# Optimization experiments

Hardware: AMD Instinct MI355X
Metric: run time of the kernel (lower is better)

The kernel has to match this reference:

```python
import jax, jax.numpy as jnp
import numpy as np

D_MODEL = 1024
HEADS = 16
D_K = D_MODEL // HEADS
B, S = 2, 2048
NEG = -1e9


def setup_inputs() -> dict:
    key = jax.random.key(0)
    ks = jax.random.split(key, 12)
    sc = 1.0 / np.sqrt(D_MODEL)
    inp = {
        'query': jax.random.normal(ks[0], (B, S, D_MODEL), jnp.float32),
        'key': jax.random.normal(ks[1], (B, S, D_MODEL), jnp.float32),
        'value': jax.random.normal(ks[2], (B, S, D_MODEL), jnp.float32),
        'mask': jnp.tril(jnp.ones((S, S), jnp.int32))[None, None],  # [1,1,S,S] causal
        'Wq': jax.random.normal(ks[3], (D_MODEL, D_MODEL), jnp.float32) * sc,
        'bq': jax.random.normal(ks[4], (D_MODEL,), jnp.float32) * 0.02,
        'Wk': jax.random.normal(ks[5], (D_MODEL, D_MODEL), jnp.float32) * sc,
        'bk': jax.random.normal(ks[6], (D_MODEL,), jnp.float32) * 0.02,
        'Wv': jax.random.normal(ks[7], (D_MODEL, D_MODEL), jnp.float32) * sc,
        'bv': jax.random.normal(ks[8], (D_MODEL,), jnp.float32) * 0.02,
        'Wo': jax.random.normal(ks[9], (D_MODEL, D_MODEL), jnp.float32) * sc,
        'bo': jax.random.normal(ks[10], (D_MODEL,), jnp.float32) * 0.02,
    }
    return inp


def reference(query, key, value, mask, Wq, bq, Wk, bk, Wv, bv, Wo, bo):
    # QKV projections (torch Linear: x @ W.T + b; here W stored as [in,out])
    def split_heads(x):  # [B,S,D] -> [B,H,S,dk]
        return x.reshape(B, S, HEADS, D_K).transpose(0, 2, 1, 3)

    q = split_heads(query @ Wq + bq)
    k = split_heads(key @ Wk + bk)
    v = split_heads(value @ Wv + bv)

    scores = jnp.einsum('bhqd,bhkd->bhqk', q, k) / np.sqrt(D_K)
    scores = jnp.where(mask == 0, NEG, scores)
    attn = jax.nn.softmax(scores, axis=-1)  # dropout p=0 (eval) -> identity
    out = jnp.einsum('bhqk,bhkd->bhqd', attn, v)
    out = out.transpose(0, 2, 1, 3).reshape(B, S, D_MODEL)
    return out @ Wo + bo
```

## Files before the change

kernel.cpp:

```cpp
#include <hip/hip_runtime.h>
#include <hip/hip_bf16.h>
#include <cstdint>
#include <cstddef>

typedef short short8 __attribute__((ext_vector_type(8)));
typedef float f32x4 __attribute__((ext_vector_type(4)));
typedef float f32x16 __attribute__((ext_vector_type(16)));

#define SS 2048
#define DK 64
#define LAMBDA 0.18033688011112042f

__device__ __forceinline__ float b2f(ushort u) {
    union { uint32_t i; float f; } x; x.i = ((uint32_t)u) << 16; return x.f;
}
__device__ __forceinline__ ushort f2b(float f) {
    union { float f; uint32_t i; } x; x.f = f;
    uint32_t r = (x.i + 0x7fffu + ((x.i >> 16) & 1u)) >> 16;
    return (ushort)r;
}
__device__ __forceinline__ uint32_t pk_bf16(float a, float b) {
    union { __hip_bfloat162 v; uint32_t u; } x;
    float2 f2; f2.x = a; f2.y = b;
    x.v = __float22bfloat162_rn(f2);
    return x.u;
}

__device__ __forceinline__ void gl_lds16(const ushort* __restrict__ g, ushort* l) {
    __builtin_amdgcn_global_load_lds(
        (const __attribute__((address_space(1))) uint32_t*)(uintptr_t)g,
        (__attribute__((address_space(3))) uint32_t*)(uintptr_t)l, 16, 0, 0);
}

__device__ __forceinline__ bool probe_bf16(const uint32_t* __restrict__ probe) {
    const int lane = threadIdx.x & 63;
    int c = 0;
#pragma unroll
    for (int i = 0; i < 4; ++i) {
        uint32_t u = probe[lane * 4 + i];
        uint32_t e = (u >> 7) & 0xffu;
        c += (e >= 100u && e <= 140u) ? 1 : 0;
    }
    unsigned long long b = __ballot(c >= 3);
    return __popcll(b) > 32;
}

__device__ __forceinline__ void ld8_f32_to_bf16(ushort* dst, const float* __restrict__ src) {
    float4 a = *(const float4*)src;
    float4 b = *(const float4*)(src + 4);
    ushort t[8] = {f2b(a.x), f2b(a.y), f2b(a.z), f2b(a.w),
                   f2b(b.x), f2b(b.y), f2b(b.z), f2b(b.w)};
    *(uint4*)dst = *(uint4*)t;
}

__global__ __launch_bounds__(256) void transpose_all(const void* __restrict__ W0,
                                                     const void* __restrict__ W1,
                                                     const void* __restrict__ W2,
                                                     const void* __restrict__ W3,
                                                     ushort* __restrict__ ws,
                                                     const uint32_t* __restrict__ probe,
                                                     size_t wotOff) {
    __shared__ __align__(16) ushort t[64 * 72];
    const bool isbf = probe_bf16(probe);
    const int z = blockIdx.z;
    const void* W = (z == 0) ? W0 : (z == 1) ? W1 : (z == 2) ? W2 : W3;
    ushort* T = ws + ((z < 3) ? ((size_t)z << 20) : wotOff);

    const int n0 = blockIdx.x * 64, k0 = blockIdx.y * 64;
    const int tid = threadIdx.x;
    const int r = tid >> 3, cg = (tid & 7) * 8;
    if (isbf) {
        const ushort* Wb = (const ushort*)W;
#pragma unroll
        for (int p = 0; p < 2; ++p) {
            int k = r + p * 32;
            *(uint4*)&t[k * 72 + cg] = *(const uint4*)&Wb[(size_t)(k0 + k) * 1024 + n0 + cg];
        }
    } else {
        const float* Wf = (const float*)W;
#pragma unroll
        for (int p = 0; p < 2; ++p) {
            int k = r + p * 32;
            ld8_f32_to_bf16(&t[k * 72 + cg], &Wf[(size_t)(k0 + k) * 1024 + n0 + cg]);
        }
    }
    __syncthreads();
#pragma unroll
    for (int p = 0; p < 2; ++p) {
        int n = r + p * 32;
        uint4 o;
        ushort* op = (ushort*)&o;
#pragma unroll
        for (int i = 0; i < 8; ++i) op[i] = t[(cg + i) * 72 + n];
        *(uint4*)&T[(size_t)(n0 + n) * 1024 + k0 + cg] = o;
    }
}

__global__ __launch_bounds__(256) void conv_qkv(const void* __restrict__ q,
                                                const void* __restrict__ k,
                                                const void* __restrict__ v,
                                                ushort* __restrict__ ws,
                                                const uint32_t* __restrict__ probe,
                                                size_t dstOff) {
    const bool isbf = probe_bf16(probe);
    const int z = blockIdx.y;
    const void* src = (z == 0) ? q : (z == 1) ? k : v;
    ushort* dst = ws + dstOff + ((size_t)z << 22);
    const size_t i = ((size_t)blockIdx.x * 256 + threadIdx.x) * 8;
    if (isbf)
        *(uint4*)&dst[i] = *(const uint4*)&((const ushort*)src)[i];
    else
        ld8_f32_to_bf16(&dst[i], &((const float*)src)[i]);
}

template <int PRE>
__global__ __launch_bounds__(256) void qkv_gemm(const void* __restrict__ qp,
                                                const void* __restrict__ kp,
                                                const void* __restrict__ vp,
                                                const void* __restrict__ bqp,
                                                const void* __restrict__ bkp,
                                                const void* __restrict__ bvp,
                                                ushort* __restrict__ ws,
                                                const uint32_t* __restrict__ probe) {
    __shared__ __align__(16) ushort As[2][128 * 32];
    __shared__ __align__(16) ushort Bs[2][128 * 32];
    const bool isbf = probe_bf16(probe);
    const int z = blockIdx.z;
    const ushort* Bt = ws + ((size_t)z << 20);
    const void* bias = (z == 0) ? bqp : (z == 1) ? bkp : bvp;
    ushort* C = ws + ((size_t)((PRE ? 16 : 5) + 4 * z) << 20);
    const float scl = (z == 0) ? LAMBDA : 1.0f;

    const int tid = threadIdx.x;
    const int lane = tid & 63, wid = tid >> 6;
    const int l15 = lane & 15, g = lane >> 4;
    const int wm = wid >> 1, wn = wid & 1;
    const int id0 = blockIdx.y * 8 + blockIdx.x;
    const int id = (id0 & 7) * 32 + (id0 >> 3);
    const int m0 = (id >> 3) * 128, n0 = (id & 7) * 128;
    const int sr = tid >> 2, sc = (tid & 3) * 8;
    const int lrow = (lane >> 2), lcol = (lane & 3) * 8;

    f32x4 acc[4][4];
#pragma unroll
    for (int i = 0; i < 4; ++i)
#pragma unroll
        for (int j = 0; j < 4; ++j) {
            f32x4 zz = {0.f, 0.f, 0.f, 0.f};
            acc[i][j] = zz;
        }

    auto stageAB = [&](int kk, int bsel) {
#pragma unroll
        for (int q = 0; q < 2; ++q) {
            const int row = (wid * 2 + q) * 16 + lrow;
            gl_lds16(&Bt[(size_t)(n0 + row) * 1024 + kk + lcol], &Bs[bsel][(wid * 2 + q) * 512]);
        }
        if (PRE) {
            const ushort* Ab = ws + ((size_t)(4 + 4 * z) << 20);
#pragma unroll
            for (int q = 0; q < 2; ++q) {
                const int row = (wid * 2 + q) * 16 + lrow;
                gl_lds16(&Ab[(size_t)(m0 + row) * 1024 + kk + lcol],
                         &As[bsel][(wid * 2 + q) * 512]);
            }
        } else {
            const void* A = (z == 0) ? qp : (z == 1) ? kp : vp;
            if (isbf) {
                const ushort* Ab = (const ushort*)A;
#pragma unroll
                for (int q = 0; q < 2; ++q) {
                    const int row = (wid * 2 + q) * 16 + lrow;
                    gl_lds16(&Ab[(size_t)(m0 + row) * 1024 + kk + lcol],
                             &As[bsel][(wid * 2 + q) * 512]);
                }
            } else {
                const float* Af = (const float*)A;
                ld8_f32_to_bf16(&As[bsel][sr * 32 + sc], &Af[(size_t)(m0 + sr) * 1024 + kk + sc]);
                ld8_f32_to_bf16(&As[bsel][(sr + 64) * 32 + sc],
                                &Af[(size_t)(m0 + sr + 64) * 1024 + kk + sc]);
            }
        }
    };

    stageAB(0, 0);
    __syncthreads();
#pragma unroll 2
    for (int kk = 0; kk < 1024; kk += 32) {
        const int cur = (kk >> 5) & 1;
        if (kk < 1024 - 32) stageAB(kk + 32, cur ^ 1);
        short8 a[4], b[4];
#pragma unroll
        for (int i = 0; i < 4; ++i)
            a[i] = *(const short8*)&As[cur][(wm * 64 + i * 16 + l15) * 32 + g * 8];
#pragma unroll
        for (int j = 0; j < 4; ++j)
            b[j] = *(const short8*)&Bs[cur][(wn * 64 + j * 16 + l15) * 32 + g * 8];
#pragma unroll
        for (int i = 0; i < 4; ++i)
#pragma unroll
            for (int j = 0; j < 4; ++j)
                acc[i][j] = __builtin_amdgcn_mfma_f32_16x16x32_bf16(a[i], b[j], acc[i][j], 0, 0, 0);
        __syncthreads();
    }

#pragma unroll
    for (int i = 0; i < 4; ++i)
#pragma unroll
        for (int j = 0; j < 4; ++j) {
            const int col = n0 + wn * 64 + j * 16 + l15;
            const float bv = isbf ? b2f(((const ushort*)bias)[col]) : ((const float*)bias)[col];
#pragma unroll
            for (int r = 0; r < 4; ++r) {
                const int row = m0 + wm * 64 + i * 16 + g * 4 + r;
                const float v = (acc[i][j][r] + bv) * scl;
                size_t idx;
                if (z != 2) {
                    idx = ((size_t)((row >> 11) * 16 + (col >> 6)) * SS + (row & 2047)) * 64 +
                          (col & 63);
                } else {
                    idx = ((size_t)((row >> 11) * 16 + (col >> 6)) * 64 + (col & 63)) * SS +
                          (row & 2047);
                }
                C[idx] = f2b(v);
            }
        }
}

__global__ __launch_bounds__(256) void out_gemm(const ushort* __restrict__ A,
                                                const ushort* __restrict__ Bt,
                                                const void* __restrict__ bias,
                                                void* __restrict__ C,
                                                const uint32_t* __restrict__ probe) {
    __shared__ __align__(16) ushort As[2][64 * 32];
    __shared__ __align__(16) ushort Bs[2][128 * 32];
    const bool isbf = probe_bf16(probe);
    const int tid = threadIdx.x;
    const int lane = tid & 63, wid = tid >> 6;
    const int l15 = lane & 15, g = lane >> 4;
    const int wm = wid >> 1, wn = wid & 1;
    const int id0 = blockIdx.y * 8 + blockIdx.x;
    const int id = (id0 & 7) * 64 + (id0 >> 3);
    const int m0 = (id >> 3) * 64, n0 = (id & 7) * 128;
    const int lrow = (lane >> 2), lcol = (lane & 3) * 8;

    f32x4 acc[2][4];
#pragma unroll
    for (int i = 0; i < 2; ++i)
#pragma unroll
        for (int j = 0; j < 4; ++j) {
            f32x4 zz = {0.f, 0.f, 0.f, 0.f};
            acc[i][j] = zz;
        }

    auto stageAB = [&](int kk, int bsel) {
        {
            const int row = wid * 16 + lrow;
            gl_lds16(&A[(size_t)(m0 + row) * 1024 + kk + lcol], &As[bsel][wid * 512]);
        }
#pragma unroll
        for (int q = 0; q < 2; ++q) {
            const int row = (wid * 2 + q) * 16 + lrow;
            gl_lds16(&Bt[(size_t)(n0 + row) * 1024 + kk + lcol], &Bs[bsel][(wid * 2 + q) * 512]);
        }
    };

    stageAB(0, 0);
    __syncthreads();
#pragma unroll 2
    for (int kk = 0; kk < 1024; kk += 32) {
        const int cur = (kk >> 5) & 1;
        if (kk < 1024 - 32) stageAB(kk + 32, cur ^ 1);
        short8 a[2], b[4];
#pragma unroll
        for (int i = 0; i < 2; ++i)
            a[i] = *(const short8*)&As[cur][(wm * 32 + i * 16 + l15) * 32 + g * 8];
#pragma unroll
        for (int j = 0; j < 4; ++j)
            b[j] = *(const short8*)&Bs[cur][(wn * 64 + j * 16 + l15) * 32 + g * 8];
#pragma unroll
        for (int i = 0; i < 2; ++i)
#pragma unroll
            for (int j = 0; j < 4; ++j)
                acc[i][j] = __builtin_amdgcn_mfma_f32_16x16x32_bf16(a[i], b[j], acc[i][j], 0, 0, 0);
        __syncthreads();
    }

#pragma unroll
    for (int i = 0; i < 2; ++i)
#pragma unroll
        for (int j = 0; j < 4; ++j) {
            const int col = n0 + wn * 64 + j * 16 + l15;
            const float bv = isbf ? b2f(((const ushort*)bias)[col]) : ((const float*)bias)[col];
#pragma unroll
            for (int r = 0; r < 4; ++r) {
                const int row = m0 + wm * 32 + i * 16 + g * 4 + r;
                const float v = acc[i][j][r] + bv;
                const size_t idx = (size_t)row * 1024 + col;
                if (isbf)
                    ((ushort*)C)[idx] = f2b(v);
                else
                    ((float*)C)[idx] = v;
            }
        }
}

__global__ __launch_bounds__(256, 2) void attn_fwd(const ushort* __restrict__ Q,
                                                   const ushort* __restrict__ K,
                                                   const ushort* __restrict__ Vt,
                                                   ushort* __restrict__ O) {
    __shared__ __align__(16) ushort Ks[2][64 * 64];
    __shared__ __align__(16) ushort Vs[2][64 * 64];

    const int y = blockIdx.y;
    const int s0i = (blockIdx.x + y) & 15;
    const int t = (y & 16) ? (15 - s0i) : s0i;
    const int tid = threadIdx.x;
    const int lane = tid & 63, wid = tid >> 6;
    const int l31 = lane & 31, h = lane >> 5;

    const ushort* Qb = Q + (size_t)y * SS * DK;
    const ushort* Kb = K + (size_t)y * SS * DK;
    const ushort* Vb = Vt + (size_t)y * DK * SS;
    const int b = y >> 4, hh = y & 15;

    const int q0w = t * 128 + wid * 32;
    const int nkt = 2 * t + 2;

    const int srow = lane >> 3;
    const int sgc = ((lane & 7) ^ srow) * 8;

    short8 qf[4];
#pragma unroll
    for (int k4 = 0; k4 < 4; ++k4)
        qf[k4] = *(const short8*)&Qb[(size_t)(q0w + l31) * 64 + k4 * 16 + h * 8];

    int foff[2][4];
#pragma unroll
    for (int aa = 0; aa < 2; ++aa)
#pragma unroll
        for (int k4 = 0; k4 < 4; ++k4)
            foff[aa][k4] = (aa * 32 + l31) * 64 + (((k4 * 2 + h) ^ (l31 & 7)) * 8);

    f32x16 acc[2];
#pragma unroll
    for (int nt = 0; nt < 2; ++nt)
#pragma unroll
        for (int r = 0; r < 16; ++r) acc[nt][r] = 0.f;
    float lpA = 0.f, lpB = 0.f;

#pragma unroll
    for (int i = 0; i < 2; ++i) {
        const int chunk = wid * 2 + i;
        const int row = chunk * 8 + srow;
        gl_lds16(&Kb[(size_t)row * 64 + sgc], &Ks[0][chunk * 512]);
        gl_lds16(&Vb[(size_t)row * SS + sgc], &Vs[0][chunk * 512]);
    }
    __syncthreads();

#pragma unroll 1
    for (int kt = 0; kt < nkt; ++kt) {
        const int cur = kt & 1;
        if (kt + 1 < nkt) {
            const int k0n = (kt + 1) * 64;
#pragma unroll
            for (int i = 0; i < 2; ++i) {
                const int chunk = wid * 2 + i;
                const int row = chunk * 8 + srow;
                gl_lds16(&Kb[(size_t)(k0n + row) * 64 + sgc], &Ks[cur ^ 1][chunk * 512]);
                gl_lds16(&Vb[(size_t)row * SS + k0n + sgc], &Vs[cur ^ 1][chunk * 512]);
            }
        }

        if (q0w + 31 >= kt * 64) {
            f32x16 sc[2];
#pragma unroll
            for (int st = 0; st < 2; ++st)
#pragma unroll
                for (int r = 0; r < 16; ++r) sc[st][r] = 0.f;
#pragma unroll
            for (int st = 0; st < 2; ++st)
#pragma unroll
                for (int k4 = 0; k4 < 4; ++k4) {
                    short8 kb = *(const short8*)&Ks[cur][foff[st][k4]];
                    sc[st] = __builtin_amdgcn_mfma_f32_32x32x16_bf16(kb, qf[k4], sc[st], 0, 0, 0);
                }

            if (kt >= nkt - 2) {
                const int qg = q0w + l31;
#pragma unroll
                for (int st = 0; st < 2; ++st)
#pragma unroll
                    for (int r = 0; r < 16; ++r) {
                        const int kvg = kt * 64 + st * 32 + (r & 3) + 8 * (r >> 2) + 4 * h;
                        if (kvg > qg) sc[st][r] = -1e9f;
                    }
            }

            uint32_t pk8[2][8];
#pragma unroll
            for (int st = 0; st < 2; ++st) {
                float ls = 0.f;
#pragma unroll
                for (int i = 0; i < 8; ++i) {
                    const float p0 = exp2f(sc[st][2 * i]);
                    const float p1 = exp2f(sc[st][2 * i + 1]);
                    ls += p0 + p1;
                    pk8[st][i] = pk_bf16(p0, p1);
                }
                if (st == 0) lpA += ls; else lpB += ls;
            }

#pragma unroll
            for (int st = 0; st < 2; ++st) {
                asm("v_permlane32_swap_b32 %0, %1" : "+v"(pk8[st][0]), "+v"(pk8[st][2]));
                asm("v_permlane32_swap_b32 %0, %1" : "+v"(pk8[st][1]), "+v"(pk8[st][3]));
                asm("v_permlane32_swap_b32 %0, %1" : "+v"(pk8[st][4]), "+v"(pk8[st][6]));
                asm("v_permlane32_swap_b32 %0, %1" : "+v"(pk8[st][5]), "+v"(pk8[st][7]));
            }

#pragma unroll
            for (int ktv = 0; ktv < 4; ++ktv) {
                union { uint32_t u[4]; short8 s; } pa;
#pragma unroll
                for (int w4 = 0; w4 < 4; ++w4) pa.u[w4] = pk8[ktv >> 1][(ktv & 1) * 4 + w4];
#pragma unroll
                for (int nt = 0; nt < 2; ++nt) {
                    short8 vb = *(const short8*)&Vs[cur][foff[nt][ktv]];
                    acc[nt] =
                        __builtin_amdgcn_mfma_f32_32x32x16_bf16(pa.s, vb, acc[nt], 0, 0, 0);
                }
            }
        }

        __syncthreads();
    }

    const float lp = lpA + lpB;
    const float lt = lp + __shfl_xor(lp, 32);
    const float inv = 1.0f / lt;
#pragma unroll
    for (int r = 0; r < 16; ++r) {
        const int qrow = (r & 3) + 8 * (r >> 2) + 4 * h;
        const float ivr = __shfl(inv, qrow);
        const int rowg = q0w + qrow;
#pragma unroll
        for (int nt = 0; nt < 2; ++nt) {
            const int col = hh * 64 + nt * 32 + l31;
            O[(size_t)(b * SS + rowg) * 1024 + col] = f2b(acc[nt][r] * ivr);
        }
    }
}

extern "C" void kernel_launch(void* const* d_in, const int* in_sizes, int n_in,
                              void* d_out, int out_size, void* d_ws, size_t ws_size,
                              hipStream_t stream) {
    const void* q = d_in[0];
    const void* k = d_in[1];
    const void* v = d_in[2];
    const void* Wq = d_in[4];
    const void* bq = d_in[5];
    const void* Wk = d_in[6];
    const void* bk = d_in[7];
    const void* Wv = d_in[8];
    const void* bv = d_in[9];
    const void* Wo = d_in[10];
    const void* bo = d_in[11];
    const uint32_t* probe = (const uint32_t*)d_in[0];

    ushort* ws = (ushort*)d_ws;
    const size_t M = (size_t)1 << 20;
    const bool pre = ws_size >= 28 * M * sizeof(ushort);

    if (pre) {
        transpose_all<<<dim3(16, 16, 4), 256, 0, stream>>>(Wq, Wk, Wv, Wo, ws, probe, 3 * M);
        conv_qkv<<<dim3(2048, 3), 256, 0, stream>>>(q, k, v, ws, probe, 4 * M);
        qkv_gemm<1><<<dim3(8, 32, 3), 256, 0, stream>>>(q, k, v, bq, bk, bv, ws, probe);
        attn_fwd<<<dim3(16, 32), 256, 0, stream>>>(ws + 16 * M, ws + 20 * M, ws + 24 * M,
                                                   ws + 4 * M);
        out_gemm<<<dim3(8, 64), 256, 0, stream>>>(ws + 4 * M, ws + 3 * M, bo, d_out, probe);
    } else {
        transpose_all<<<dim3(16, 16, 4), 256, 0, stream>>>(Wq, Wk, Wv, Wo, ws, probe, 4 * M);
        qkv_gemm<0><<<dim3(8, 32, 3), 256, 0, stream>>>(q, k, v, bq, bk, bv, ws, probe);
        attn_fwd<<<dim3(16, 32), 256, 0, stream>>>(ws + 5 * M, ws + 9 * M, ws + 13 * M, ws);
        out_gemm<<<dim3(8, 64), 256, 0, stream>>>(ws, ws + 4 * M, bo, d_out, probe);
    }
}
```

Measured before the change: 230.4 us.

## Triple-buffer LDS in GEMMs with partial vmcnt waits for deeper prefetch

Moves the pre-converted QKV GEMM path and the output projection GEMM from double to triple LDS buffering, issuing loads two K-steps ahead. The full __syncthreads is replaced with s_waitcnt vmcnt(N) plus s_barrier, so only the oldest stage has to land before each iteration. The goal is to hide global-to-LDS latency behind the MFMA work. The extra buffer raises shared memory per block and launch_bounds(256,3) caps registers, which may limit occupancy or cause spills. The hand-counted vmcnt values must match the exact number of outstanding loads per stage or the results will be wrong.

```diff
diff --git a/kernel.cpp b/kernel.cpp
--- a/kernel.cpp
+++ b/kernel.cpp
@@ -114,16 +114,16 @@
 }
 
 template <int PRE>
-__global__ __launch_bounds__(256) void qkv_gemm(const void* __restrict__ qp,
-                                                const void* __restrict__ kp,
-                                                const void* __restrict__ vp,
-                                                const void* __restrict__ bqp,
-                                                const void* __restrict__ bkp,
-                                                const void* __restrict__ bvp,
-                                                ushort* __restrict__ ws,
-                                                const uint32_t* __restrict__ probe) {
-    __shared__ __align__(16) ushort As[2][128 * 32];
-    __shared__ __align__(16) ushort Bs[2][128 * 32];
+__global__ __launch_bounds__(256, 3) void qkv_gemm(const void* __restrict__ qp,
+                                                   const void* __restrict__ kp,
+                                                   const void* __restrict__ vp,
+                                                   const void* __restrict__ bqp,
+                                                   const void* __restrict__ bkp,
+                                                   const void* __restrict__ bvp,
+                                                   ushort* __restrict__ ws,
+                                                   const uint32_t* __restrict__ probe) {
+    __shared__ __align__(16) ushort As[3][128 * 32];
+    __shared__ __align__(16) ushort Bs[3][128 * 32];
     const bool isbf = probe_bf16(probe);
     const int z = blockIdx.z;
     const ushort* Bt = ws + ((size_t)z << 20);
@@ -150,21 +150,59 @@
             acc[i][j] = zz;
         }
 
-    auto stageAB = [&](int kk, int bsel) {
-#pragma unroll
-        for (int q = 0; q < 2; ++q) {
-            const int row = (wid * 2 + q) * 16 + lrow;
-            gl_lds16(&Bt[(size_t)(n0 + row) * 1024 + kk + lcol], &Bs[bsel][(wid * 2 + q) * 512]);
-        }
-        if (PRE) {
-            const ushort* Ab = ws + ((size_t)(4 + 4 * z) << 20);
+    if (PRE) {
+        const ushort* Ab = ws + ((size_t)(4 + 4 * z) << 20);
+        auto stage1 = [&](int kk, int bsel) {
 #pragma unroll
             for (int q = 0; q < 2; ++q) {
                 const int row = (wid * 2 + q) * 16 + lrow;
+                gl_lds16(&Bt[(size_t)(n0 + row) * 1024 + kk + lcol],
+                         &Bs[bsel][(wid * 2 + q) * 512]);
                 gl_lds16(&Ab[(size_t)(m0 + row) * 1024 + kk + lcol],
                          &As[bsel][(wid * 2 + q) * 512]);
             }
-        } else {
+        };
+        stage1(0, 0);
+        stage1(32, 1);
+        asm volatile("s_waitcnt vmcnt(4)" ::: "memory");
+        __builtin_amdgcn_s_barrier();
+        __builtin_amdgcn_sched_barrier(0);
+        int cur = 0;
+#pragma unroll 1
+        for (int kk = 0; kk < 1024; kk += 32) {
+            const int nxt = (cur >= 1) ? cur - 1 : cur + 2;
+            if (kk + 64 < 1024) stage1(kk + 64, nxt);
+            short8 a[4], b[4];
+#pragma unroll
+            for (int i = 0; i < 4; ++i)
+                a[i] = *(const short8*)&As[cur][(wm * 64 + i * 16 + l15) * 32 + g * 8];
+#pragma unroll
+            for (int j = 0; j < 4; ++j)
+                b[j] = *(const short8*)&Bs[cur][(wn * 64 + j * 16 + l15) * 32 + g * 8];
+#pragma unroll
+            for (int i = 0; i < 4; ++i)
+#pragma unroll
+                for (int j = 0; j < 4; ++j)
+                    acc[i][j] =
+                        __builtin_amdgcn_mfma_f32_16x16x32_bf16(a[i], b[j], acc[i][j], 0, 0, 0);
+            if (kk + 32 < 1024) {
+                if (kk + 64 < 1024)
+                    asm volatile("s_waitcnt vmcnt(4)" ::: "memory");
+                else
+                    asm volatile("s_waitcnt vmcnt(0)" ::: "memory");
+                __builtin_amdgcn_s_barrier();
+                __builtin_amdgcn_sched_barrier(0);
+            }
+            cur = (cur == 2) ? 0 : cur + 1;
+        }
+    } else {
+        auto stageAB = [&](int kk, int bsel) {
+#pragma unroll
+            for (int q = 0; q < 2; ++q) {
+                const int row = (wid * 2 + q) * 16 + lrow;
+                gl_lds16(&Bt[(size_t)(n0 + row) * 1024 + kk + lcol],
+                         &Bs[bsel][(wid * 2 + q) * 512]);
+            }
             const void* A = (z == 0) ? qp : (z == 1) ? kp : vp;
             if (isbf) {
                 const ushort* Ab = (const ushort*)A;
@@ -180,28 +218,28 @@
                 ld8_f32_to_bf16(&As[bsel][(sr + 64) * 32 + sc],
                                 &Af[(size_t)(m0 + sr + 64) * 1024 + kk + sc]);
             }
-        }
-    };
-
-    stageAB(0, 0);
-    __syncthreads();
+        };
+        stageAB(0, 0);
+        __syncthreads();
 #pragma unroll 2
-    for (int kk = 0; kk < 1024; kk += 32) {
-        const int cur = (kk >> 5) & 1;
-        if (kk < 1024 - 32) stageAB(kk + 32, cur ^ 1);
-        short8 a[4], b[4];
-#pragma unroll
-        for (int i = 0; i < 4; ++i)
-            a[i] = *(const short8*)&As[cur][(wm * 64 + i * 16 + l15) * 32 + g * 8];
-#pragma unroll
-        for (int j = 0; j < 4; ++j)
-            b[j] = *(const short8*)&Bs[cur][(wn * 64 + j * 16 + l15) * 32 + g * 8];
-#pragma unroll
-        for (int i = 0; i < 4; ++i)
+        for (int kk = 0; kk < 1024; kk += 32) {
+            const int cur = (kk >> 5) & 1;
+            if (kk < 1024 - 32) stageAB(kk + 32, cur ^ 1);
+            short8 a[4], b[4];
+#pragma unroll
+            for (int i = 0; i < 4; ++i)
+                a[i] = *(const short8*)&As[cur][(wm * 64 + i * 16 + l15) * 32 + g * 8];
 #pragma unroll
             for (int j = 0; j < 4; ++j)
-                acc[i][j] = __builtin_amdgcn_mfma_f32_16x16x32_bf16(a[i], b[j], acc[i][j], 0, 0, 0);
-        __syncthreads();
+                b[j] = *(const short8*)&Bs[cur][(wn * 64 + j * 16 + l15) * 32 + g * 8];
+#pragma unroll
+            for (int i = 0; i < 4; ++i)
+#pragma unroll
+                for (int j = 0; j < 4; ++j)
+                    acc[i][j] =
+                        __builtin_amdgcn_mfma_f32_16x16x32_bf16(a[i], b[j], acc[i][j], 0, 0, 0);
+            __syncthreads();
+        }
     }
 
 #pragma unroll
@@ -232,8 +270,8 @@
                                                 const void* __restrict__ bias,
                                                 void* __restrict__ C,
                                                 const uint32_t* __restrict__ probe) {
-    __shared__ __align__(16) ushort As[2][64 * 32];
-    __shared__ __align__(16) ushort Bs[2][128 * 32];
+    __shared__ __align__(16) ushort As[3][64 * 32];
+    __shared__ __align__(16) ushort Bs[3][128 * 32];
     const bool isbf = probe_bf16(probe);
     const int tid = threadIdx.x;
     const int lane = tid & 63, wid = tid >> 6;
@@ -253,7 +291,7 @@
             acc[i][j] = zz;
         }
 
-    auto stageAB = [&](int kk, int bsel) {
+    auto stage1 = [&](int kk, int bsel) {
         {
             const int row = wid * 16 + lrow;
             gl_lds16(&A[(size_t)(m0 + row) * 1024 + kk + lcol], &As[bsel][wid * 512]);
@@ -265,12 +303,16 @@
         }
     };
 
-    stageAB(0, 0);
-    __syncthreads();
-#pragma unroll 2
+    stage1(0, 0);
+    stage1(32, 1);
+    asm volatile("s_waitcnt vmcnt(3)" ::: "memory");
+    __builtin_amdgcn_s_barrier();
+    __builtin_amdgcn_sched_barrier(0);
+    int cur = 0;
+#pragma unroll 1
     for (int kk = 0; kk < 1024; kk += 32) {
-        const int cur = (kk >> 5) & 1;
-        if (kk < 1024 - 32) stageAB(kk + 32, cur ^ 1);
+        const int nxt = (cur >= 1) ? cur - 1 : cur + 2;
+        if (kk + 64 < 1024) stage1(kk + 64, nxt);
         short8 a[2], b[4];
 #pragma unroll
         for (int i = 0; i < 2; ++i)
@@ -283,7 +325,15 @@
 #pragma unroll
             for (int j = 0; j < 4; ++j)
                 acc[i][j] = __builtin_amdgcn_mfma_f32_16x16x32_bf16(a[i], b[j], acc[i][j], 0, 0, 0);
-        __syncthreads();
+        if (kk + 32 < 1024) {
+            if (kk + 64 < 1024)
+                asm volatile("s_waitcnt vmcnt(3)" ::: "memory");
+            else
+                asm volatile("s_waitcnt vmcnt(0)" ::: "memory");
+            __builtin_amdgcn_s_barrier();
+            __builtin_amdgcn_sched_barrier(0);
+        }
+        cur = (cur == 2) ? 0 : cur + 1;
     }
 
 #pragma unroll
```

Measured after the change: 233.1 us. About the same (+1.2%).
